# Kernel optimization log

Measured on AMD Instinct MI355X. Metric: run time of the kernel, lower is better.

The kernel has to match this reference:

```python
import jax, jax.numpy as jnp
import numpy as np

NEG_SLOPE = 0.2
N_NODES = 50000
N_EDGES = 800000
IN_DIM = 256
HID_DIM = 256
HEADS = 8
HEAD_DIM = HID_DIM // HEADS


def setup_inputs() -> dict:
    key = jax.random.key(0)
    ks = jax.random.split(key, 12)
    def glorot(k, shape):
        fan = sum(shape[-2:]) if len(shape) > 1 else shape[-1] + 1
        return jax.random.normal(k, shape, jnp.float32) * jnp.sqrt(2.0 / fan)
    return {
        "data": jax.random.normal(ks[0], (N_NODES, IN_DIM), jnp.float32),
        "src": jax.random.randint(ks[1], (N_EDGES,), 0, N_NODES),
        "dst": jax.random.randint(ks[2], (N_EDGES,), 0, N_NODES),
        "W1": glorot(ks[3], (IN_DIM, HID_DIM)),
        "al1": glorot(ks[4], (HEADS, HEAD_DIM)),
        "ar1": glorot(ks[5], (HEADS, HEAD_DIM)),
        "b1": jnp.zeros((HID_DIM,), jnp.float32),
        "W2": glorot(ks[6], (HID_DIM, HID_DIM)),
        "al2": glorot(ks[7], (HEADS, HEAD_DIM)),
        "ar2": glorot(ks[8], (HEADS, HEAD_DIM)),
        "b2": jnp.zeros((HID_DIM,), jnp.float32),
    }


def gat_layer(x, src, dst, W, al, ar, b):
    """One DGL-style GATConv layer with ReLU activation."""
    N = x.shape[0]
    feat = (x @ W).reshape(N, HEADS, HEAD_DIM)            # [N,H,D]
    el = jnp.sum(feat * al[None], axis=-1)                # [N,H]
    er = jnp.sum(feat * ar[None], axis=-1)                # [N,H]
    e = el[src] + er[dst]                                  # [E,H]
    e = jnp.where(e > 0, e, NEG_SLOPE * e)                 # LeakyReLU(0.2)
    # segment softmax over incoming edges of each dst node
    m = jax.ops.segment_max(e, dst, num_segments=N)        # [N,H] (-inf for empty)
    a = jnp.exp(e - m[dst])                                # [E,H]
    denom = jax.ops.segment_sum(a, dst, num_segments=N)    # [N,H]
    alpha = a / denom[dst]                                 # [E,H]
    msg = feat[src] * alpha[:, :, None]                    # [E,H,D]
    out = jax.ops.segment_sum(msg, dst, num_segments=N)    # [N,H,D]
    out = out + b.reshape(1, HEADS, HEAD_DIM)
    out = jax.nn.relu(out)
    return out.reshape(N, HID_DIM)


def reference(data, src, dst, W1, al1, ar1, b1, W2, al2, ar2, b2):
    h = gat_layer(data, src, dst, W1, al1, ar1, b1)
    h = gat_layer(h, src, dst, W2, al2, ar2, b2)
    return h
```

## Files before the change

### kernel.cpp

```cpp
#include <hip/hip_runtime.h>

#define N_NODES 50000
#define N_EDGES 800000
#define DIM 256
#define HEADS 8
#define NEG_SLOPE 0.2f

typedef unsigned short u16;
typedef float floatx4 __attribute__((ext_vector_type(4)));
typedef __bf16 bf16x8 __attribute__((ext_vector_type(8)));

__device__ __forceinline__ float b2f(u16 u) {
    union { unsigned int i; float f; } v; v.i = ((unsigned int)u) << 16; return v.f;
}
__device__ __forceinline__ u16 f2b(float f) {
    union { float f; unsigned int i; } v; v.f = f;
    unsigned int x = v.i;
    if ((x & 0x7f800000u) == 0x7f800000u && (x & 0x007fffffu)) {
        return (u16)((x >> 16) | 0x0040u);
    }
    unsigned int r = (x + 0x7fffu + ((x >> 16) & 1u)) >> 16;
    return (u16)r;
}

__global__ __launch_bounds__(256) void fill_u32(unsigned int* __restrict__ p,
                                                unsigned int v, int n) {
    int i = blockIdx.x * 256 + threadIdx.x;
    if (i < n) p[i] = v;
}

__global__ __launch_bounds__(256) void init_kernel(const unsigned int* __restrict__ d,
                                                   int* __restrict__ counts,
                                                   int* __restrict__ flag) {
    int i = blockIdx.x * 256 + threadIdx.x;
    if (i < N_NODES) counts[i] = 0;
    if (blockIdx.x == 0) {
        __shared__ int cnt;
        if (threadIdx.x == 0) cnt = 0;
        __syncthreads();
        unsigned int w = d[threadIdx.x];
        int bad = 0;
        #pragma unroll
        for (int half = 0; half < 2; ++half) {
            u16 u = (u16)(w >> (16 * half));
            unsigned int e = (u >> 7) & 0xFFu;
            if (u != 0 && (e >= 141u || e <= 27u)) bad = 1;
        }
        atomicAdd(&cnt, bad);
        __syncthreads();
        if (threadIdx.x == 0) *flag = (cnt > 64) ? 1 : 0;
    }
}

__global__ __launch_bounds__(256) void prep_kernel(const void* __restrict__ W1,
                                                   const void* __restrict__ W2,
                                                   const void* __restrict__ data,
                                                   u16* __restrict__ Wt1,
                                                   u16* __restrict__ Wt2,
                                                   u16* __restrict__ datab,
                                                   const int* __restrict__ flagp) {
    const int isf = *flagp;
    int b = blockIdx.x;
    if (b < 32) {
        const void* W = (b < 16) ? W1 : W2;
        u16* Wt = (b < 16) ? Wt1 : Wt2;
        int t = b & 15;
        int k0 = (t >> 2) * 64, n0 = (t & 3) * 64;
        __shared__ float lt[64][65];
        int c = threadIdx.x & 63, r0 = threadIdx.x >> 6;
        #pragma unroll
        for (int j = 0; j < 16; ++j) {
            int r = j * 4 + r0;
            lt[r][c] = isf ? ((const float*)W)[(k0 + r) * 256 + n0 + c]
                           : b2f(((const u16*)W)[(k0 + r) * 256 + n0 + c]);
        }
        __syncthreads();
        #pragma unroll
        for (int j = 0; j < 16; ++j) {
            int rn = j * 4 + r0;
            Wt[(n0 + rn) * 256 + k0 + c] = f2b(lt[c][rn]);
        }
    } else {
        if (!isf) return;
        int base = (b - 32) * 2048 + threadIdx.x * 8;
        const float* df = (const float*)data + base;
        float4 f0 = *(const float4*)df;
        float4 f1 = *(const float4*)(df + 4);
        u16 tb[8] = {f2b(f0.x), f2b(f0.y), f2b(f0.z), f2b(f0.w),
                     f2b(f1.x), f2b(f1.y), f2b(f1.z), f2b(f1.w)};
        *(uint4*)(datab + base) = *(uint4*)tb;
    }
}

__global__ __launch_bounds__(256) void hist_kernel(const int* __restrict__ dst,
                                                   int* __restrict__ counts, int E) {
    int i = blockIdx.x * 256 + threadIdx.x;
    if (i < E) atomicAdd(&counts[dst[i]], 1);
}

__global__ __launch_bounds__(256) void scan_partial(const int* __restrict__ counts,
                                                    int* __restrict__ partial, int n) {
    int b = blockIdx.x, tid = threadIdx.x;
    int base = b * 1024 + tid * 4;
    int s = 0;
    #pragma unroll
    for (int k = 0; k < 4; ++k) if (base + k < n) s += counts[base + k];
    int lane = tid & 63;
    #pragma unroll
    for (int off = 32; off; off >>= 1) s += __shfl_xor(s, off);
    __shared__ int wsum[4];
    if (lane == 0) wsum[tid >> 6] = s;
    __syncthreads();
    if (tid == 0) partial[b] = wsum[0] + wsum[1] + wsum[2] + wsum[3];
}

__global__ __launch_bounds__(64) void scan_offsets(const int* __restrict__ partial,
                                                   int* __restrict__ offsets,
                                                   int* __restrict__ row_ptr,
                                                   int nb, int n) {
    int t = threadIdx.x;
    int v0 = (t < nb) ? partial[t] : 0;
    int v = v0;
    #pragma unroll
    for (int d = 1; d < 64; d <<= 1) {
        int u = __shfl_up(v, d);
        if (t >= d) v += u;
    }
    if (t < nb) offsets[t] = v - v0;
    if (t == 63) row_ptr[n] = v;
}

__global__ __launch_bounds__(256) void scan_write(const int* __restrict__ counts,
                                                  const int* __restrict__ offsets,
                                                  int* __restrict__ row_ptr,
                                                  int* __restrict__ wptr, int n) {
    int b = blockIdx.x, tid = threadIdx.x;
    int base = b * 1024 + tid * 4;
    int v[4]; int s = 0;
    #pragma unroll
    for (int k = 0; k < 4; ++k) { v[k] = (base + k < n) ? counts[base + k] : 0; s += v[k]; }
    int lane = tid & 63, w = tid >> 6;
    int incl = s;
    #pragma unroll
    for (int d = 1; d < 64; d <<= 1) {
        int u = __shfl_up(incl, d);
        if (lane >= d) incl += u;
    }
    __shared__ int wsum[4];
    if (lane == 63) wsum[w] = incl;
    __syncthreads();
    int woff = 0;
    for (int i = 0; i < w; ++i) woff += wsum[i];
    int run = offsets[b] + woff + incl - s;
    #pragma unroll
    for (int k = 0; k < 4; ++k) {
        if (base + k < n) { row_ptr[base + k] = run; wptr[base + k] = run; run += v[k]; }
    }
}

__global__ __launch_bounds__(256) void scatter_kernel(const int* __restrict__ src,
                                                      const int* __restrict__ dst,
                                                      int* __restrict__ wptr,
                                                      int* __restrict__ src_sorted, int E) {
    int i = blockIdx.x * 256 + threadIdx.x;
    if (i < E) {
        int pos = atomicAdd(&wptr[dst[i]], 1);
        src_sorted[pos] = src[i];
    }
}

#define LDA 264
#define LDB 40

__global__ __launch_bounds__(256, 2) void gemm_fused(const u16* __restrict__ Aisf,
                                                     const u16* __restrict__ Abf,
                                                     const u16* __restrict__ Wt,
                                                     u16* __restrict__ outF,
                                                     float* __restrict__ el,
                                                     float* __restrict__ er,
                                                     const void* __restrict__ al,
                                                     const void* __restrict__ ar,
                                                     int M, const int* __restrict__ flagp) {
    const int isf = *flagp;
    const u16* A = isf ? Aisf : Abf;
    __shared__ u16 As[64][LDA];
    __shared__ u16 Ws[256][LDB];
    const int tid  = threadIdx.x;
    const int w    = tid >> 6;
    const int lane = tid & 63;
    const int quad = lane >> 4;
    const int l16  = lane & 15;
    const int m0   = blockIdx.x * 64;

    #pragma unroll
    for (int it = 0; it < 8; ++it) {
        int idx = it * 256 + tid;
        int r = idx >> 5;
        int c = (idx & 31) << 3;
        int gr = m0 + r;
        if (gr < M) {
            *(uint4*)&As[r][c] = *(const uint4*)(A + gr * 256 + c);
        } else {
            uint4 z = {0u, 0u, 0u, 0u};
            *(uint4*)&As[r][c] = z;
        }
    }

    floatx4 acc[4][4] = {};

    for (int s = 0; s < 8; ++s) {
        __syncthreads();
        #pragma unroll
        for (int it = 0; it < 4; ++it) {
            int idx = it * 256 + tid;
            int n = idx >> 2;
            int k8 = (idx & 3) << 3;
            *(uint4*)&Ws[n][k8] = *(const uint4*)(Wt + n * 256 + s * 32 + k8);
        }
        __syncthreads();

        bf16x8 af[4], bfv[4];
        #pragma unroll
        for (int i = 0; i < 4; ++i)
            af[i] = *(const bf16x8*)&As[16 * i + l16][s * 32 + quad * 8];
        #pragma unroll
        for (int t = 0; t < 4; ++t)
            bfv[t] = *(const bf16x8*)&Ws[64 * w + 16 * t + l16][quad * 8];
        #pragma unroll
        for (int i = 0; i < 4; ++i)
            #pragma unroll
            for (int t = 0; t < 4; ++t)
                acc[i][t] = __builtin_amdgcn_mfma_f32_16x16x32_bf16(af[i], bfv[t], acc[i][t], 0, 0, 0);
    }

    #pragma unroll
    for (int i = 0; i < 4; ++i)
        #pragma unroll
        for (int t = 0; t < 4; ++t)
            #pragma unroll
            for (int r = 0; r < 4; ++r) {
                int row = m0 + 16 * i + quad * 4 + r;
                if (row < M) outF[row * 256 + 64 * w + 16 * t + l16] = f2b(acc[i][t][r]);
            }

    float alv[4], arv[4];
    #pragma unroll
    for (int t = 0; t < 4; ++t) {
        int c = 64 * w + 16 * t + l16;
        alv[t] = isf ? ((const float*)al)[c] : b2f(((const u16*)al)[c]);
        arv[t] = isf ? ((const float*)ar)[c] : b2f(((const u16*)ar)[c]);
    }
    #pragma unroll
    for (int i = 0; i < 4; ++i)
        #pragma unroll
        for (int r = 0; r < 4; ++r) {
            int row = m0 + 16 * i + quad * 4 + r;
            #pragma unroll
            for (int tt = 0; tt < 2; ++tt) {
                float pl = acc[i][2 * tt][r] * alv[2 * tt] + acc[i][2 * tt + 1][r] * alv[2 * tt + 1];
                float pr = acc[i][2 * tt][r] * arv[2 * tt] + acc[i][2 * tt + 1][r] * arv[2 * tt + 1];
                #pragma unroll
                for (int mask = 1; mask <= 8; mask <<= 1) {
                    pl += __shfl_xor(pl, mask);
                    pr += __shfl_xor(pr, mask);
                }
                if (l16 == 0 && row < M) {
                    el[row * 8 + 2 * w + tt] = pl;
                    er[row * 8 + 2 * w + tt] = pr;
                }
            }
        }
}

__global__ __launch_bounds__(256) void aggregate_kernel(const u16* __restrict__ feat,
                                                        const float* __restrict__ el,
                                                        const float* __restrict__ er,
                                                        const void* __restrict__ bias,
                                                        const int* __restrict__ row_ptr,
                                                        const int* __restrict__ src_sorted,
                                                        void* __restrict__ out,
                                                        int out_mode,
                                                        const int* __restrict__ flagp) {
    const int isf = *flagp;
    const int lane = threadIdx.x & 63;
    const int node = blockIdx.x * 4 + (threadIdx.x >> 6);
    if (node >= N_NODES) return;
    const int h = lane >> 3;
    const int j = lane & 7;
    const int beg = row_ptr[node];
    const int deg = row_ptr[node + 1] - beg;
    const float ern = er[node * HEADS + h];

    float m0v = -1e30f, ss0 = 0.f;
    float m1v = -1e30f, ss1 = 0.f;
    for (int i = j; i < deg; i += 16) {
        int s0 = src_sorted[beg + i];
        int i2 = i + 8;
        int s1 = (i2 < deg) ? src_sorted[beg + i2] : 0;
        float e0 = el[s0 * 8 + h] + ern;
        float e1 = el[s1 * 8 + h] + ern;
        e0 = e0 > 0.f ? e0 : NEG_SLOPE * e0;
        e1 = e1 > 0.f ? e1 : NEG_SLOPE * e1;
        if (i2 >= deg) e1 = -3e30f;
        float mn0 = fmaxf(m0v, e0);
        ss0 = ss0 * __expf(m0v - mn0) + __expf(e0 - mn0);
        m0v = mn0;
        float mn1 = fmaxf(m1v, e1);
        ss1 = ss1 * __expf(m1v - mn1) + __expf(e1 - mn1);
        m1v = mn1;
    }
    float m = fmaxf(m0v, m1v);
    float ssum = ss0 * __expf(m0v - m) + ss1 * __expf(m1v - m);
    #pragma unroll
    for (int mask = 1; mask <= 4; mask <<= 1) {
        float mo = __shfl_xor(m, mask);
        float so = __shfl_xor(ssum, mask);
        float mn = fmaxf(m, mo);
        ssum = ssum * __expf(m - mn) + so * __expf(mo - mn);
        m = mn;
    }
    const float mx = m;
    const float inv = ssum > 0.f ? 1.f / ssum : 0.f;

    const int q = lane & 31;
    const int half = lane >> 5;
    const int hq = q >> 2;
    float a[8] = {};

    int sC = 0; float avC = 0.f;
    if (j < deg) {
        sC = src_sorted[beg + j];
        float e = el[sC * 8 + h] + ern;
        e = e > 0.f ? e : NEG_SLOPE * e;
        avC = __expf(e - mx) * inv;
    }
    uint4 f[4]; float ae[4];
    #pragma unroll
    for (int u = 0; u < 4; ++u) {
        int sel = hq * 8 + 2 * u + half;
        int se = __shfl(sC, sel);
        ae[u] = __shfl(avC, sel);
        f[u] = *(const uint4*)(feat + (size_t)se * DIM + 8 * q);
    }

    #pragma unroll 2
    for (int c0 = 0; c0 < deg; c0 += 8) {
        uint4 f2[4]; float ae2[4];
        {
            int sN = 0; float avN = 0.f;
            int i = c0 + 8 + j;
            if (i < deg) {
                sN = src_sorted[beg + i];
                float e = el[sN * 8 + h] + ern;
                e = e > 0.f ? e : NEG_SLOPE * e;
                avN = __expf(e - mx) * inv;
            }
            #pragma unroll
            for (int u = 0; u < 4; ++u) {
                int sel = hq * 8 + 2 * u + half;
                int se = __shfl(sN, sel);
                ae2[u] = __shfl(avN, sel);
                f2[u] = *(const uint4*)(feat + (size_t)se * DIM + 8 * q);
            }
        }
        #pragma unroll
        for (int u = 0; u < 4; ++u) {
            float w = ae[u];
            a[0] += w * b2f((u16)(f[u].x & 0xffffu)); a[1] += w * b2f((u16)(f[u].x >> 16));
            a[2] += w * b2f((u16)(f[u].y & 0xffffu)); a[3] += w * b2f((u16)(f[u].y >> 16));
            a[4] += w * b2f((u16)(f[u].z & 0xffffu)); a[5] += w * b2f((u16)(f[u].z >> 16));
            a[6] += w * b2f((u16)(f[u].w & 0xffffu)); a[7] += w * b2f((u16)(f[u].w >> 16));
        }
        #pragma unroll
        for (int u = 0; u < 4; ++u) { f[u] = f2[u]; ae[u] = ae2[u]; }
    }

    #pragma unroll
    for (int k = 0; k < 8; ++k) a[k] += __shfl_xor(a[k], 32);

    if (half == 0) {
        float o[8];
        if (isf) {
            float4 b0 = *(const float4*)((const float*)bias + 8 * q);
            float4 b1 = *(const float4*)((const float*)bias + 8 * q + 4);
            o[0] = a[0] + b0.x; o[1] = a[1] + b0.y; o[2] = a[2] + b0.z; o[3] = a[3] + b0.w;
            o[4] = a[4] + b1.x; o[5] = a[5] + b1.y; o[6] = a[6] + b1.z; o[7] = a[7] + b1.w;
        } else {
            uint4 bu = *(const uint4*)((const u16*)bias + 8 * q);
            o[0] = a[0] + b2f((u16)(bu.x & 0xffffu)); o[1] = a[1] + b2f((u16)(bu.x >> 16));
            o[2] = a[2] + b2f((u16)(bu.y & 0xffffu)); o[3] = a[3] + b2f((u16)(bu.y >> 16));
            o[4] = a[4] + b2f((u16)(bu.z & 0xffffu)); o[5] = a[5] + b2f((u16)(bu.z >> 16));
            o[6] = a[6] + b2f((u16)(bu.w & 0xffffu)); o[7] = a[7] + b2f((u16)(bu.w >> 16));
        }
        #pragma unroll
        for (int k = 0; k < 8; ++k) o[k] = fmaxf(o[k], 0.f);
        if (out_mode == 0 || !isf) {
            u16 pk[8] = {f2b(o[0]), f2b(o[1]), f2b(o[2]), f2b(o[3]),
                         f2b(o[4]), f2b(o[5]), f2b(o[6]), f2b(o[7])};
            *(uint4*)((u16*)out + (size_t)node * DIM + 8 * q) = *(uint4*)pk;
        } else {
            float4 v0 = {o[0], o[1], o[2], o[3]};
            float4 v1 = {o[4], o[5], o[6], o[7]};
            *(float4*)((float*)out + (size_t)node * DIM + 8 * q) = v0;
            *(float4*)((float*)out + (size_t)node * DIM + 8 * q + 4) = v1;
        }
    }
}

extern "C" void kernel_launch(void* const* d_in, const int* in_sizes, int n_in,
                              void* d_out, int out_size, void* d_ws, size_t ws_size,
                              hipStream_t stream) {
    const void* data = d_in[0];
    const int* src = (const int*)d_in[1];
    const int* dst = (const int*)d_in[2];
    const void* W1  = d_in[3];
    const void* al1 = d_in[4];
    const void* ar1 = d_in[5];
    const void* b1  = d_in[6];
    const void* W2  = d_in[7];
    const void* al2 = d_in[8];
    const void* ar2 = d_in[9];
    const void* b2  = d_in[10];

    const size_t NEEDED =
        (size_t)N_NODES * DIM * 2 +
        (size_t)N_NODES * HEADS * 4 * 2 +
        (size_t)N_NODES * 4 * 2 +
        (size_t)(N_NODES + 4) * 4 +
        (size_t)N_EDGES * 4 +
        2 * 256 * 256 * 2 +
        1024;

    if (ws_size < NEEDED) {
        int nwords = (out_size + 1) / 2;
        fill_u32<<<(nwords + 255) / 256, 256, 0, stream>>>(
            (unsigned int*)d_out, 0x42C842C8u, nwords);
        return;
    }

    char* ws = (char*)d_ws;
    u16* feat = (u16*)ws;        ws += (size_t)N_NODES * DIM * 2;
    float* el = (float*)ws;      ws += (size_t)N_NODES * HEADS * 4;
    float* er = (float*)ws;      ws += (size_t)N_NODES * HEADS * 4;
    int* counts = (int*)ws;      ws += (size_t)N_NODES * 4;
    int* wptr = (int*)ws;        ws += (size_t)N_NODES * 4;
    int* row_ptr = (int*)ws;     ws += (size_t)(N_NODES + 4) * 4;
    int* src_sorted = (int*)ws;  ws += (size_t)N_EDGES * 4;
    u16* Wt1 = (u16*)ws;         ws += 256 * 256 * 2;
    u16* Wt2 = (u16*)ws;         ws += 256 * 256 * 2;
    int* partial = (int*)ws;     ws += 256;
    int* offsets = (int*)ws;     ws += 256;
    int* flag = (int*)ws;        ws += 256;

    u16* h1    = (u16*)d_out;
    u16* datab = (u16*)d_out + (size_t)N_NODES * DIM;

    const int nb = (N_NODES + 1023) / 1024;

    init_kernel<<<(N_NODES + 255) / 256, 256, 0, stream>>>(
        (const unsigned int*)data, counts, flag);
    prep_kernel<<<32 + (N_NODES * DIM) / 2048, 256, 0, stream>>>(
        W1, W2, data, Wt1, Wt2, datab, flag);
    hist_kernel<<<(N_EDGES + 255) / 256, 256, 0, stream>>>(dst, counts, N_EDGES);
    scan_partial<<<nb, 256, 0, stream>>>(counts, partial, N_NODES);
    scan_offsets<<<1, 64, 0, stream>>>(partial, offsets, row_ptr, nb, N_NODES);
    scan_write<<<nb, 256, 0, stream>>>(counts, offsets, row_ptr, wptr, N_NODES);
    scatter_kernel<<<(N_EDGES + 255) / 256, 256, 0, stream>>>(src, dst, wptr, src_sorted, N_EDGES);

    const int gemm_blocks = (N_NODES + 63) / 64;
    const int agg_blocks = (N_NODES + 3) / 4;

    gemm_fused<<<gemm_blocks, 256, 0, stream>>>(datab, (const u16*)data, Wt1, feat,
                                                el, er, al1, ar1, N_NODES, flag);
    aggregate_kernel<<<agg_blocks, 256, 0, stream>>>(feat, el, er, b1, row_ptr, src_sorted,
                                                     (void*)h1, 0, flag);
    gemm_fused<<<gemm_blocks, 256, 0, stream>>>(h1, h1, Wt2, feat,
                                                el, er, al2, ar2, N_NODES, flag);
    aggregate_kernel<<<agg_blocks, 256, 0, stream>>>(feat, el, er, b2, row_ptr, src_sorted,
                                                     d_out, 2, flag);
}
```

Measured before the change: 437.3 us.

## Fuse input fp32-to-bf16 conversion into GEMM and read weights directly from global

The separate pass that converted the fp32 input features to bf16 is removed. The first GEMM now loads fp32 rows and converts them to bf16 while staging them into LDS, which avoids writing and re-reading a 25 MB intermediate. The weight tile is no longer staged through shared memory each k-step. Each lane reads its B fragments straight from the L2-resident transposed weights, which drops two barriers per step and the Ws buffer. The launch-bounds occupancy hint is raised from 2 to 4 blocks, at the cost of more uncoalesced global loads for weights and tighter register limits.

```diff
diff --git a/kernel.cpp b/kernel.cpp
--- a/kernel.cpp
+++ b/kernel.cpp
@@ -54,41 +54,28 @@
 
 __global__ __launch_bounds__(256) void prep_kernel(const void* __restrict__ W1,
                                                    const void* __restrict__ W2,
-                                                   const void* __restrict__ data,
                                                    u16* __restrict__ Wt1,
                                                    u16* __restrict__ Wt2,
-                                                   u16* __restrict__ datab,
                                                    const int* __restrict__ flagp) {
     const int isf = *flagp;
     int b = blockIdx.x;
-    if (b < 32) {
-        const void* W = (b < 16) ? W1 : W2;
-        u16* Wt = (b < 16) ? Wt1 : Wt2;
-        int t = b & 15;
-        int k0 = (t >> 2) * 64, n0 = (t & 3) * 64;
-        __shared__ float lt[64][65];
-        int c = threadIdx.x & 63, r0 = threadIdx.x >> 6;
-        #pragma unroll
-        for (int j = 0; j < 16; ++j) {
-            int r = j * 4 + r0;
-            lt[r][c] = isf ? ((const float*)W)[(k0 + r) * 256 + n0 + c]
-                           : b2f(((const u16*)W)[(k0 + r) * 256 + n0 + c]);
-        }
-        __syncthreads();
-        #pragma unroll
-        for (int j = 0; j < 16; ++j) {
-            int rn = j * 4 + r0;
-            Wt[(n0 + rn) * 256 + k0 + c] = f2b(lt[c][rn]);
-        }
-    } else {
-        if (!isf) return;
-        int base = (b - 32) * 2048 + threadIdx.x * 8;
-        const float* df = (const float*)data + base;
-        float4 f0 = *(const float4*)df;
-        float4 f1 = *(const float4*)(df + 4);
-        u16 tb[8] = {f2b(f0.x), f2b(f0.y), f2b(f0.z), f2b(f0.w),
-                     f2b(f1.x), f2b(f1.y), f2b(f1.z), f2b(f1.w)};
-        *(uint4*)(datab + base) = *(uint4*)tb;
+    const void* W = (b < 16) ? W1 : W2;
+    u16* Wt = (b < 16) ? Wt1 : Wt2;
+    int t = b & 15;
+    int k0 = (t >> 2) * 64, n0 = (t & 3) * 64;
+    __shared__ float lt[64][65];
+    int c = threadIdx.x & 63, r0 = threadIdx.x >> 6;
+    #pragma unroll
+    for (int j = 0; j < 16; ++j) {
+        int r = j * 4 + r0;
+        lt[r][c] = isf ? ((const float*)W)[(k0 + r) * 256 + n0 + c]
+                       : b2f(((const u16*)W)[(k0 + r) * 256 + n0 + c]);
+    }
+    __syncthreads();
+    #pragma unroll
+    for (int j = 0; j < 16; ++j) {
+        int rn = j * 4 + r0;
+        Wt[(n0 + rn) * 256 + k0 + c] = f2b(lt[c][rn]);
     }
 }
 
@@ -170,10 +157,9 @@
 }
 
 #define LDA 264
-#define LDB 40
-
-__global__ __launch_bounds__(256, 2) void gemm_fused(const u16* __restrict__ Aisf,
-                                                     const u16* __restrict__ Abf,
+
+__global__ __launch_bounds__(256, 4) void gemm_fused(const void* __restrict__ Araw,
+                                                     int maybe_f32,
                                                      const u16* __restrict__ Wt,
                                                      u16* __restrict__ outF,
                                                      float* __restrict__ el,
@@ -182,9 +168,8 @@
                                                      const void* __restrict__ ar,
                                                      int M, const int* __restrict__ flagp) {
     const int isf = *flagp;
-    const u16* A = isf ? Aisf : Abf;
+    const bool af32 = (maybe_f32 != 0) && (isf != 0);
     __shared__ u16 As[64][LDA];
-    __shared__ u16 Ws[256][LDB];
     const int tid  = threadIdx.x;
     const int w    = tid >> 6;
     const int lane = tid & 63;
@@ -192,40 +177,55 @@
     const int l16  = lane & 15;
     const int m0   = blockIdx.x * 64;
 
-    #pragma unroll
-    for (int it = 0; it < 8; ++it) {
-        int idx = it * 256 + tid;
-        int r = idx >> 5;
-        int c = (idx & 31) << 3;
-        int gr = m0 + r;
-        if (gr < M) {
-            *(uint4*)&As[r][c] = *(const uint4*)(A + gr * 256 + c);
-        } else {
-            uint4 z = {0u, 0u, 0u, 0u};
-            *(uint4*)&As[r][c] = z;
-        }
-    }
+    if (af32) {
+        const float* Af = (const float*)Araw;
+        #pragma unroll
+        for (int it = 0; it < 8; ++it) {
+            int idx = it * 256 + tid;
+            int r = idx >> 5;
+            int c = (idx & 31) << 3;
+            int gr = m0 + r;
+            u16 tb[8];
+            if (gr < M) {
+                float4 f0 = *(const float4*)(Af + (size_t)gr * 256 + c);
+                float4 f1 = *(const float4*)(Af + (size_t)gr * 256 + c + 4);
+                tb[0] = f2b(f0.x); tb[1] = f2b(f0.y); tb[2] = f2b(f0.z); tb[3] = f2b(f0.w);
+                tb[4] = f2b(f1.x); tb[5] = f2b(f1.y); tb[6] = f2b(f1.z); tb[7] = f2b(f1.w);
+            } else {
+                #pragma unroll
+                for (int k = 0; k < 8; ++k) tb[k] = 0;
+            }
+            *(uint4*)&As[r][c] = *(uint4*)tb;
+        }
+    } else {
+        const u16* Ab = (const u16*)Araw;
+        #pragma unroll
+        for (int it = 0; it < 8; ++it) {
+            int idx = it * 256 + tid;
+            int r = idx >> 5;
+            int c = (idx & 31) << 3;
+            int gr = m0 + r;
+            if (gr < M) {
+                *(uint4*)&As[r][c] = *(const uint4*)(Ab + (size_t)gr * 256 + c);
+            } else {
+                uint4 z = {0u, 0u, 0u, 0u};
+                *(uint4*)&As[r][c] = z;
+            }
+        }
+    }
+    __syncthreads();
 
     floatx4 acc[4][4] = {};
+    const u16* wbase = Wt + (size_t)(64 * w + l16) * 256 + quad * 8;
 
     for (int s = 0; s < 8; ++s) {
-        __syncthreads();
-        #pragma unroll
-        for (int it = 0; it < 4; ++it) {
-            int idx = it * 256 + tid;
-            int n = idx >> 2;
-            int k8 = (idx & 3) << 3;
-            *(uint4*)&Ws[n][k8] = *(const uint4*)(Wt + n * 256 + s * 32 + k8);
-        }
-        __syncthreads();
-
         bf16x8 af[4], bfv[4];
+        #pragma unroll
+        for (int t = 0; t < 4; ++t)
+            bfv[t] = *(const bf16x8*)(wbase + (size_t)t * 16 * 256 + s * 32);
         #pragma unroll
         for (int i = 0; i < 4; ++i)
             af[i] = *(const bf16x8*)&As[16 * i + l16][s * 32 + quad * 8];
-        #pragma unroll
-        for (int t = 0; t < 4; ++t)
-            bfv[t] = *(const bf16x8*)&Ws[64 * w + 16 * t + l16][quad * 8];
         #pragma unroll
         for (int i = 0; i < 4; ++i)
             #pragma unroll
@@ -240,7 +240,7 @@
             #pragma unroll
             for (int r = 0; r < 4; ++r) {
                 int row = m0 + 16 * i + quad * 4 + r;
-                if (row < M) outF[row * 256 + 64 * w + 16 * t + l16] = f2b(acc[i][t][r]);
+                if (row < M) outF[(size_t)row * 256 + 64 * w + 16 * t + l16] = f2b(acc[i][t][r]);
             }
 
     float alv[4], arv[4];
@@ -365,11 +365,11 @@
         }
         #pragma unroll
         for (int u = 0; u < 4; ++u) {
-            float w = ae[u];
-            a[0] += w * b2f((u16)(f[u].x & 0xffffu)); a[1] += w * b2f((u16)(f[u].x >> 16));
-            a[2] += w * b2f((u16)(f[u].y & 0xffffu)); a[3] += w * b2f((u16)(f[u].y >> 16));
-            a[4] += w * b2f((u16)(f[u].z & 0xffffu)); a[5] += w * b2f((u16)(f[u].z >> 16));
-            a[6] += w * b2f((u16)(f[u].w & 0xffffu)); a[7] += w * b2f((u16)(f[u].w >> 16));
+            float wgt = ae[u];
+            a[0] += wgt * b2f((u16)(f[u].x & 0xffffu)); a[1] += wgt * b2f((u16)(f[u].x >> 16));
+            a[2] += wgt * b2f((u16)(f[u].y & 0xffffu)); a[3] += wgt * b2f((u16)(f[u].y >> 16));
+            a[4] += wgt * b2f((u16)(f[u].z & 0xffffu)); a[5] += wgt * b2f((u16)(f[u].z >> 16));
+            a[6] += wgt * b2f((u16)(f[u].w & 0xffffu)); a[7] += wgt * b2f((u16)(f[u].w >> 16));
         }
         #pragma unroll
         for (int u = 0; u < 4; ++u) { f[u] = f2[u]; ae[u] = ae2[u]; }
@@ -452,15 +452,13 @@
     int* offsets = (int*)ws;     ws += 256;
     int* flag = (int*)ws;        ws += 256;
 
-    u16* h1    = (u16*)d_out;
-    u16* datab = (u16*)d_out + (size_t)N_NODES * DIM;
+    u16* h1 = (u16*)d_out;
 
     const int nb = (N_NODES + 1023) / 1024;
 
     init_kernel<<<(N_NODES + 255) / 256, 256, 0, stream>>>(
         (const unsigned int*)data, counts, flag);
-    prep_kernel<<<32 + (N_NODES * DIM) / 2048, 256, 0, stream>>>(
-        W1, W2, data, Wt1, Wt2, datab, flag);
+    prep_kernel<<<32, 256, 0, stream>>>(W1, W2, Wt1, Wt2, flag);
     hist_kernel<<<(N_EDGES + 255) / 256, 256, 0, stream>>>(dst, counts, N_EDGES);
     scan_partial<<<nb, 256, 0, stream>>>(counts, partial, N_NODES);
     scan_offsets<<<1, 64, 0, stream>>>(partial, offsets, row_ptr, nb, N_NODES);
@@ -470,11 +468,11 @@
     const int gemm_blocks = (N_NODES + 63) / 64;
     const int agg_blocks = (N_NODES + 3) / 4;
 
-    gemm_fused<<<gemm_blocks, 256, 0, stream>>>(datab, (const u16*)data, Wt1, feat,
+    gemm_fused<<<gemm_blocks, 256, 0, stream>>>(data, 1, Wt1, feat,
                                                 el, er, al1, ar1, N_NODES, flag);
     aggregate_kernel<<<agg_blocks, 256, 0, stream>>>(feat, el, er, b1, row_ptr, src_sorted,
                                                      (void*)h1, 0, flag);
-    gemm_fused<<<gemm_blocks, 256, 0, stream>>>(h1, h1, Wt2, feat,
+    gemm_fused<<<gemm_blocks, 256, 0, stream>>>(h1, 0, Wt2, feat,
                                                 el, er, al2, ar2, N_NODES, flag);
     aggregate_kernel<<<agg_blocks, 256, 0, stream>>>(feat, el, er, b2, row_ptr, src_sorted,
                                                      d_out, 2, flag);
```

Result: faster. 419.1 us (-4.2%).
